# Performance work log

Hardware: AMD Instinct MI355X
Metric: run time of the kernel (lower is better)

Reference implementation:

```python
import jax, jax.numpy as jnp
import numpy as np

N_NODES = 100000
N_EDGES = 1600000
D_IN = 128
D_HID = 128
D_OUT = 128


def setup_inputs() -> dict:
    key = jax.random.key(0)
    ks = jax.random.split(key, 12)
    x = jax.random.normal(ks[0], (N_NODES, D_IN), dtype=jnp.float32)
    src = jax.random.randint(ks[1], (N_EDGES,), 0, N_NODES, dtype=jnp.int32)
    dst = jax.random.randint(ks[2], (N_EDGES,), 0, N_NODES, dtype=jnp.int32)
    s = 0.05
    # layer 0: in->hid, layer 1: hid->hid, layer 2: hid->out
    Wl0 = jax.random.normal(ks[3], (D_HID, D_IN), dtype=jnp.float32) * s
    bl0 = jnp.zeros((D_HID,), dtype=jnp.float32)
    Wr0 = jax.random.normal(ks[4], (D_HID, D_IN), dtype=jnp.float32) * s
    Wl1 = jax.random.normal(ks[5], (D_HID, D_HID), dtype=jnp.float32) * s
    bl1 = jnp.zeros((D_HID,), dtype=jnp.float32)
    Wr1 = jax.random.normal(ks[6], (D_HID, D_HID), dtype=jnp.float32) * s
    Wl2 = jax.random.normal(ks[7], (D_OUT, D_HID), dtype=jnp.float32) * s
    bl2 = jnp.zeros((D_OUT,), dtype=jnp.float32)
    Wr2 = jax.random.normal(ks[8], (D_OUT, D_HID), dtype=jnp.float32) * s
    return {"x": x, "src": src, "dst": dst,
            "Wl0": Wl0, "bl0": bl0, "Wr0": Wr0,
            "Wl1": Wl1, "bl1": bl1, "Wr1": Wr1,
            "Wl2": Wl2, "bl2": bl2, "Wr2": Wr2}


def _sage_conv(h, src, dst, Wl, bl, Wr, n_nodes):
    # mean aggregation over incoming neighbors: out_i = mean_{j: (j->i)} h_j
    msg = jax.ops.segment_sum(h[src], dst, num_segments=n_nodes)  # [N, d_in]
    deg = jax.ops.segment_sum(jnp.ones(dst.shape, dtype=h.dtype), dst, num_segments=n_nodes)
    agg = msg / jnp.maximum(deg, 1.0)[:, None]
    # PyG SAGEConv: lin_l(agg) (with bias) + lin_r(h) (root, no bias)
    return agg @ Wl.T + bl + h @ Wr.T


def reference(x, src, dst, Wl0, bl0, Wr0, Wl1, bl1, Wr1, Wl2, bl2, Wr2):
    n = x.shape[0]
    # dropout is identity in eval mode
    h = jax.nn.relu(_sage_conv(x, src, dst, Wl0, bl0, Wr0, n))
    h = jax.nn.relu(_sage_conv(h, src, dst, Wl1, bl1, Wr1, n))
    return _sage_conv(h, src, dst, Wl2, bl2, Wr2, n)
```

## Files before the change

kernel.cpp:

```cpp
#include <hip/hip_runtime.h>

#define N_NODES 100000
#define N_EDGES 1600000
#define D 128
#define NBS 98

typedef __attribute__((ext_vector_type(8))) short bf16x8;
typedef __attribute__((ext_vector_type(4))) float f32x4;
typedef __attribute__((ext_vector_type(4))) unsigned int u32x4;
typedef __attribute__((ext_vector_type(2))) unsigned int u32x2;

union U16x8 { u32x4 u; bf16x8 b; };

__device__ __forceinline__ unsigned int bf16_rne_hi(float x) {
    unsigned int u = __float_as_uint(x);
    unsigned int r = u + 0x7fffu + ((u >> 16) & 1u);
    return r & 0xffff0000u;
}
__device__ __forceinline__ unsigned int pack_hilo(float x) {
    unsigned int hb = bf16_rne_hi(x);
    float hf = __uint_as_float(hb);
    unsigned int lb = bf16_rne_hi(x - hf);
    return hb | (lb >> 16);
}
__device__ __forceinline__ float unpack_val(unsigned int p) {
    return __uint_as_float(p & 0xffff0000u) + __uint_as_float(p << 16);
}


__global__ __launch_bounds__(256) void hist_kernel(const int* __restrict__ dst,
                                                   int* __restrict__ cnt, int n) {
    int i = blockIdx.x * blockDim.x + threadIdx.x;
    if (i < n) atomicAdd(&cnt[dst[i]], 1);
}

__global__ __launch_bounds__(256) void scan_reduce(const int* __restrict__ cnt,
                                                   int* __restrict__ bsum, int n) {
    __shared__ int s[4];
    int b = blockIdx.x, t = threadIdx.x;
    int base = b * 1024;
    int v = 0;
    for (int q = 0; q < 4; ++q) {
        int i = base + q * 256 + t;
        if (i < n) v += cnt[i];
    }
    for (int off = 32; off > 0; off >>= 1) v += __shfl_down(v, off, 64);
    if ((t & 63) == 0) s[t >> 6] = v;
    __syncthreads();
    if (t == 0) bsum[b] = s[0] + s[1] + s[2] + s[3];
}

__global__ __launch_bounds__(128) void scan_partials(const int* __restrict__ bsum,
                                                     int* __restrict__ bpre) {
    __shared__ int s[128];
    int t = threadIdx.x;
    int v = (t < NBS) ? bsum[t] : 0;
    s[t] = v;
    __syncthreads();
    for (int off = 1; off < 128; off <<= 1) {
        int u = (t >= off) ? s[t - off] : 0;
        __syncthreads();
        s[t] += u;
        __syncthreads();
    }
    if (t < NBS) bpre[t] = s[t] - v;
}

__global__ __launch_bounds__(1024) void scan_write(const int* __restrict__ cnt,
                                                   const int* __restrict__ bpre,
                                                   int* __restrict__ row_ptr, int n) {
    __shared__ int s[1024];
    int b = blockIdx.x, t = threadIdx.x;
    int i = b * 1024 + t;
    int c = (i < n) ? cnt[i] : 0;
    s[t] = c;
    __syncthreads();
    for (int off = 1; off < 1024; off <<= 1) {
        int u = (t >= off) ? s[t - off] : 0;
        __syncthreads();
        s[t] += u;
        __syncthreads();
    }
    if (i < n) row_ptr[i] = bpre[b] + s[t] - c;
    if (b == 0 && t == 0) row_ptr[n] = N_EDGES;
}

__global__ __launch_bounds__(256) void scatter_kernel(const int* __restrict__ src,
                                                      const int* __restrict__ dst,
                                                      const int* __restrict__ row_ptr,
                                                      int* __restrict__ cursor,
                                                      int* __restrict__ sorted_src, int n) {
    int i = blockIdx.x * blockDim.x + threadIdx.x;
    if (i < n) {
        int d = dst[i];
        int p = atomicAdd(&cursor[d], 1);
        sorted_src[row_ptr[d] + p] = src[i];
    }
}


__global__ __launch_bounds__(256) void split_x(const float* __restrict__ x,
                                               unsigned int* __restrict__ Hp) {
    int i = blockIdx.x * 256 + threadIdx.x;
    if (i >= N_NODES * 32) return;
    float4 v = reinterpret_cast<const float4*>(x)[i];
    u32x4 p;
    p.x = pack_hilo(v.x); p.y = pack_hilo(v.y);
    p.z = pack_hilo(v.z); p.w = pack_hilo(v.w);
    *reinterpret_cast<u32x4*>(Hp + (size_t)i * 4) = p;
}

__global__ __launch_bounds__(256) void split_w(const float* __restrict__ Wl,
                                               const float* __restrict__ Wr,
                                               unsigned short* __restrict__ whi,
                                               unsigned short* __restrict__ wlo) {
    int i = blockIdx.x * 256 + threadIdx.x;
    if (i >= 128 * 256) return;
    int o = i >> 8, k = i & 255;
    float v = (k < 128) ? Wl[o * 128 + k] : Wr[o * 128 + (k - 128)];
    unsigned int hb = bf16_rne_hi(v);
    whi[i] = (unsigned short)(hb >> 16);
    wlo[i] = (unsigned short)(bf16_rne_hi(v - __uint_as_float(hb)) >> 16);
}


__global__ __launch_bounds__(256) void aggregate_packed(const unsigned int* __restrict__ Hp,
                                                        const int* __restrict__ row_ptr,
                                                        const int* __restrict__ sorted_src,
                                                        unsigned int* __restrict__ Ap) {
    int wid = (blockIdx.x * blockDim.x + threadIdx.x) >> 6;
    int lane = threadIdx.x & 63;
    if (wid >= N_NODES) return;
    int beg = row_ptr[wid], end = row_ptr[wid + 1];
    int deg = end - beg;
    float a0 = 0.f, a1 = 0.f;
    int j = beg;
    for (; j + 7 < end; j += 8) {
        int s0 = sorted_src[j + 0], s1 = sorted_src[j + 1];
        int s2 = sorted_src[j + 2], s3 = sorted_src[j + 3];
        int s4 = sorted_src[j + 4], s5 = sorted_src[j + 5];
        int s6 = sorted_src[j + 6], s7 = sorted_src[j + 7];
        u32x2 p0 = *reinterpret_cast<const u32x2*>(Hp + (size_t)s0 * D + lane * 2);
        u32x2 p1 = *reinterpret_cast<const u32x2*>(Hp + (size_t)s1 * D + lane * 2);
        u32x2 p2 = *reinterpret_cast<const u32x2*>(Hp + (size_t)s2 * D + lane * 2);
        u32x2 p3 = *reinterpret_cast<const u32x2*>(Hp + (size_t)s3 * D + lane * 2);
        u32x2 p4 = *reinterpret_cast<const u32x2*>(Hp + (size_t)s4 * D + lane * 2);
        u32x2 p5 = *reinterpret_cast<const u32x2*>(Hp + (size_t)s5 * D + lane * 2);
        u32x2 p6 = *reinterpret_cast<const u32x2*>(Hp + (size_t)s6 * D + lane * 2);
        u32x2 p7 = *reinterpret_cast<const u32x2*>(Hp + (size_t)s7 * D + lane * 2);
        a0 += unpack_val(p0.x) + unpack_val(p1.x) + unpack_val(p2.x) + unpack_val(p3.x)
            + unpack_val(p4.x) + unpack_val(p5.x) + unpack_val(p6.x) + unpack_val(p7.x);
        a1 += unpack_val(p0.y) + unpack_val(p1.y) + unpack_val(p2.y) + unpack_val(p3.y)
            + unpack_val(p4.y) + unpack_val(p5.y) + unpack_val(p6.y) + unpack_val(p7.y);
    }
    for (; j < end; ++j) {
        int s = sorted_src[j];
        u32x2 p = *reinterpret_cast<const u32x2*>(Hp + (size_t)s * D + lane * 2);
        a0 += unpack_val(p.x);
        a1 += unpack_val(p.y);
    }
    float inv = 1.0f / (float)max(deg, 1);
    u32x2 o;
    o.x = pack_hilo(a0 * inv);
    o.y = pack_hilo(a1 * inv);
    *reinterpret_cast<u32x2*>(Ap + (size_t)wid * D + lane * 2) = o;
}


__global__ __launch_bounds__(512, 2) void sage_gemm_mfma(
        const unsigned int* __restrict__ Hp,
        const unsigned int* __restrict__ Ap,
        const unsigned short* __restrict__ WHI,
        const unsigned short* __restrict__ WLO,
        const float* __restrict__ bl,
        void* __restrict__ outp,
        int relu, int pack_out) {
    __shared__ short WH[32768];
    __shared__ short WLl[32768];
    int tid = threadIdx.x;

    for (int i = tid; i < 4096; i += 512) {
        int o = i >> 5, kg = i & 31;
        int sk = (kg * 8) ^ ((o & 7) << 3);
        *reinterpret_cast<bf16x8*>(&WH[o * 256 + sk]) =
            *reinterpret_cast<const bf16x8*>(WHI + o * 256 + kg * 8);
        *reinterpret_cast<bf16x8*>(&WLl[o * 256 + sk]) =
            *reinterpret_cast<const bf16x8*>(WLO + o * 256 + kg * 8);
    }
    __syncthreads();

    int w = tid >> 6, l = tid & 63;
    int lr = l & 15, lg = l >> 4;
    int sw = (lr & 7) << 3;
    int mt0 = blockIdx.x * 256 + w * 32;
    int mt1 = mt0 + 16;
    int r0 = min(mt0 + lr, N_NODES - 1);
    int r1 = min(mt1 + lr, N_NODES - 1);
    const unsigned int* a0A = Ap + (size_t)r0 * D + lg * 8;
    const unsigned int* a0H = Hp + (size_t)r0 * D + lg * 8;
    const unsigned int* a1A = Ap + (size_t)r1 * D + lg * 8;
    const unsigned int* a1H = Hp + (size_t)r1 * D + lg * 8;

    f32x4 acc0[8], acc1[8];
    #pragma unroll
    for (int nt = 0; nt < 8; ++nt) { acc0[nt] = (f32x4)0.f; acc1[nt] = (f32x4)0.f; }

    u32x4 p00 = *reinterpret_cast<const u32x4*>(a0A);
    u32x4 p01 = *reinterpret_cast<const u32x4*>(a0A + 4);
    u32x4 p10 = *reinterpret_cast<const u32x4*>(a1A);
    u32x4 p11 = *reinterpret_cast<const u32x4*>(a1A + 4);

    #pragma unroll
    for (int kk = 0; kk < 8; ++kk) {
        U16x8 h0, l0, h1, l1;
        h0.u.x = (p00.x >> 16) | (p00.y & 0xffff0000u);
        l0.u.x = (p00.x & 0xffffu) | (p00.y << 16);
        h0.u.y = (p00.z >> 16) | (p00.w & 0xffff0000u);
        l0.u.y = (p00.z & 0xffffu) | (p00.w << 16);
        h0.u.z = (p01.x >> 16) | (p01.y & 0xffff0000u);
        l0.u.z = (p01.x & 0xffffu) | (p01.y << 16);
        h0.u.w = (p01.z >> 16) | (p01.w & 0xffff0000u);
        l0.u.w = (p01.z & 0xffffu) | (p01.w << 16);
        h1.u.x = (p10.x >> 16) | (p10.y & 0xffff0000u);
        l1.u.x = (p10.x & 0xffffu) | (p10.y << 16);
        h1.u.y = (p10.z >> 16) | (p10.w & 0xffff0000u);
        l1.u.y = (p10.z & 0xffffu) | (p10.w << 16);
        h1.u.z = (p11.x >> 16) | (p11.y & 0xffff0000u);
        l1.u.z = (p11.x & 0xffffu) | (p11.y << 16);
        h1.u.w = (p11.z >> 16) | (p11.w & 0xffff0000u);
        l1.u.w = (p11.z & 0xffffu) | (p11.w << 16);
        bf16x8 a0h = h0.b, a0l = l0.b, a1h = h1.b, a1l = l1.b;

        if (kk < 7) {
            int kn = kk + 1;
            const unsigned int* s0 = (kn < 4) ? (a0A + kn * 32) : (a0H + (kn - 4) * 32);
            const unsigned int* s1 = (kn < 4) ? (a1A + kn * 32) : (a1H + (kn - 4) * 32);
            p00 = *reinterpret_cast<const u32x4*>(s0);
            p01 = *reinterpret_cast<const u32x4*>(s0 + 4);
            p10 = *reinterpret_cast<const u32x4*>(s1);
            p11 = *reinterpret_cast<const u32x4*>(s1 + 4);
        }

        int ka = (kk * 32 + lg * 8) ^ sw;
        #pragma unroll
        for (int nt = 0; nt < 8; ++nt) {
            int base = nt * 4096 + lr * 256 + ka;
            bf16x8 bh = *reinterpret_cast<const bf16x8*>(WH + base);
            bf16x8 bl_ = *reinterpret_cast<const bf16x8*>(WLl + base);
            acc0[nt] = __builtin_amdgcn_mfma_f32_16x16x32_bf16(a0h, bh, acc0[nt], 0, 0, 0);
            acc0[nt] = __builtin_amdgcn_mfma_f32_16x16x32_bf16(a0l, bh, acc0[nt], 0, 0, 0);
            acc0[nt] = __builtin_amdgcn_mfma_f32_16x16x32_bf16(a0h, bl_, acc0[nt], 0, 0, 0);
            acc1[nt] = __builtin_amdgcn_mfma_f32_16x16x32_bf16(a1h, bh, acc1[nt], 0, 0, 0);
            acc1[nt] = __builtin_amdgcn_mfma_f32_16x16x32_bf16(a1l, bh, acc1[nt], 0, 0, 0);
            acc1[nt] = __builtin_amdgcn_mfma_f32_16x16x32_bf16(a1h, bl_, acc1[nt], 0, 0, 0);
        }
    }

    #pragma unroll
    for (int nt = 0; nt < 8; ++nt) {
        int col = nt * 16 + lr;
        float bv = bl[col];
        #pragma unroll
        for (int ri = 0; ri < 4; ++ri) {
            int n0 = mt0 + lg * 4 + ri;
            if (n0 < N_NODES) {
                float v = acc0[nt][ri] + bv;
                if (relu) v = fmaxf(v, 0.f);
                if (pack_out)
                    ((unsigned int*)outp)[(size_t)n0 * D + col] = pack_hilo(v);
                else
                    ((float*)outp)[(size_t)n0 * D + col] = v;
            }
            int n1 = mt1 + lg * 4 + ri;
            if (n1 < N_NODES) {
                float v = acc1[nt][ri] + bv;
                if (relu) v = fmaxf(v, 0.f);
                if (pack_out)
                    ((unsigned int*)outp)[(size_t)n1 * D + col] = pack_hilo(v);
                else
                    ((float*)outp)[(size_t)n1 * D + col] = v;
            }
        }
    }
}


extern "C" void kernel_launch(void* const* d_in, const int* in_sizes, int n_in,
                              void* d_out, int out_size, void* d_ws, size_t ws_size,
                              hipStream_t stream) {
    const float* x   = (const float*)d_in[0];
    const int*   src = (const int*)d_in[1];
    const int*   dst = (const int*)d_in[2];
    const float* Wl0 = (const float*)d_in[3];
    const float* bl0 = (const float*)d_in[4];
    const float* Wr0 = (const float*)d_in[5];
    const float* Wl1 = (const float*)d_in[6];
    const float* bl1 = (const float*)d_in[7];
    const float* Wr1 = (const float*)d_in[8];
    const float* Wl2 = (const float*)d_in[9];
    const float* bl2 = (const float*)d_in[10];
    const float* Wr2 = (const float*)d_in[11];

    int* cnt        = (int*)d_ws;
    int* row_ptr    = cnt + 100032;
    int* sorted_src = row_ptr + 100032;
    unsigned short* W0h = (unsigned short*)((char*)d_ws + 7200256);
    unsigned short* W0l = W0h + 32768;
    unsigned short* W1h = W0l + 32768;
    unsigned short* W1l = W1h + 32768;
    unsigned short* W2h = W1l + 32768;
    unsigned short* W2l = W2h + 32768;
    unsigned int* Ap = (unsigned int*)((char*)d_ws + 7593472);
    int* bsum = (int*)W0h;
    int* bpre = bsum + 128;

    unsigned int* Hp = (unsigned int*)d_out;
    float* outf = (float*)d_out;

    const int EB = (N_EDGES + 255) / 256;
    const int GB = (N_NODES + 255) / 256;
    const int AB = (N_NODES * 64 + 255) / 256;
    const int SB = (N_NODES * 32 + 255) / 256;
    const int WB = (128 * 256 + 255) / 256;

    hipMemsetAsync(cnt, 0, N_NODES * sizeof(int), stream);
    hist_kernel<<<EB, 256, 0, stream>>>(dst, cnt, N_EDGES);
    scan_reduce<<<NBS, 256, 0, stream>>>(cnt, bsum, N_NODES);
    scan_partials<<<1, 128, 0, stream>>>(bsum, bpre);
    scan_write<<<NBS, 1024, 0, stream>>>(cnt, bpre, row_ptr, N_NODES);
    hipMemsetAsync(cnt, 0, N_NODES * sizeof(int), stream);
    scatter_kernel<<<EB, 256, 0, stream>>>(src, dst, row_ptr, cnt, sorted_src, N_EDGES);

    split_x<<<SB, 256, 0, stream>>>(x, Hp);
    split_w<<<WB, 256, 0, stream>>>(Wl0, Wr0, W0h, W0l);
    split_w<<<WB, 256, 0, stream>>>(Wl1, Wr1, W1h, W1l);
    split_w<<<WB, 256, 0, stream>>>(Wl2, Wr2, W2h, W2l);

    aggregate_packed<<<AB, 256, 0, stream>>>(Hp, row_ptr, sorted_src, Ap);
    sage_gemm_mfma<<<GB, 512, 0, stream>>>(Hp, Ap, W0h, W0l, bl0, Hp, 1, 1);
    aggregate_packed<<<AB, 256, 0, stream>>>(Hp, row_ptr, sorted_src, Ap);
    sage_gemm_mfma<<<GB, 512, 0, stream>>>(Hp, Ap, W1h, W1l, bl1, Hp, 1, 1);
    aggregate_packed<<<AB, 256, 0, stream>>>(Hp, row_ptr, sorted_src, Ap);
    sage_gemm_mfma<<<GB, 512, 0, stream>>>(Hp, Ap, W2h, W2l, bl2, outf, 0, 0);
}
```

Measured before the change: 791.2 us.

## Use feature-chunked transposed layout for aggregation to improve gather cache locality

Stores node features in 16 column chunks of 8 packed values each, laid out chunk-major, and adds an aggregation kernel that stages each block's neighbor indices in shared memory and sweeps chunks one at a time. The aim is to keep each chunk's gather working set small enough to stay cache-resident instead of randomly gathering full rows from a large array. The GEMM kernel is templated to read and write the chunked layout. The new path needs a larger workspace and falls back to the old path otherwise. Gathers become narrower, 32-byte segments per neighbor, which may reduce memory efficiency.

```diff
diff --git a/kernel.cpp b/kernel.cpp
--- a/kernel.cpp
+++ b/kernel.cpp
@@ -4,6 +4,9 @@
 #define N_EDGES 1600000
 #define D 128
 #define NBS 98
+#define NCH 16
+#define CHW 8
+#define MAXE 2048
 
 typedef __attribute__((ext_vector_type(8))) short bf16x8;
 typedef __attribute__((ext_vector_type(4))) float f32x4;
@@ -98,17 +101,6 @@
     }
 }
 
-
-__global__ __launch_bounds__(256) void split_x(const float* __restrict__ x,
-                                               unsigned int* __restrict__ Hp) {
-    int i = blockIdx.x * 256 + threadIdx.x;
-    if (i >= N_NODES * 32) return;
-    float4 v = reinterpret_cast<const float4*>(x)[i];
-    u32x4 p;
-    p.x = pack_hilo(v.x); p.y = pack_hilo(v.y);
-    p.z = pack_hilo(v.z); p.w = pack_hilo(v.w);
-    *reinterpret_cast<u32x4*>(Hp + (size_t)i * 4) = p;
-}
 
 __global__ __launch_bounds__(256) void split_w(const float* __restrict__ Wl,
                                                const float* __restrict__ Wr,
@@ -121,6 +113,97 @@
     unsigned int hb = bf16_rne_hi(v);
     whi[i] = (unsigned short)(hb >> 16);
     wlo[i] = (unsigned short)(bf16_rne_hi(v - __uint_as_float(hb)) >> 16);
+}
+
+__global__ __launch_bounds__(256) void split_x_t(const float* __restrict__ x,
+                                                 unsigned int* __restrict__ Hpt) {
+    int i = blockIdx.x * 256 + threadIdx.x;
+    if (i >= N_NODES * NCH) return;
+    int n = i >> 4, c = i & 15;
+    float4 v0 = *reinterpret_cast<const float4*>(x + (size_t)n * D + c * CHW);
+    float4 v1 = *reinterpret_cast<const float4*>(x + (size_t)n * D + c * CHW + 4);
+    u32x4 p0, p1;
+    p0.x = pack_hilo(v0.x); p0.y = pack_hilo(v0.y);
+    p0.z = pack_hilo(v0.z); p0.w = pack_hilo(v0.w);
+    p1.x = pack_hilo(v1.x); p1.y = pack_hilo(v1.y);
+    p1.z = pack_hilo(v1.z); p1.w = pack_hilo(v1.w);
+    unsigned int* o = Hpt + ((size_t)c * N_NODES + n) * CHW;
+    *reinterpret_cast<u32x4*>(o) = p0;
+    *reinterpret_cast<u32x4*>(o + 4) = p1;
+}
+
+__global__ __launch_bounds__(256) void split_x(const float* __restrict__ x,
+                                               unsigned int* __restrict__ Hp) {
+    int i = blockIdx.x * 256 + threadIdx.x;
+    if (i >= N_NODES * 32) return;
+    float4 v = reinterpret_cast<const float4*>(x)[i];
+    u32x4 p;
+    p.x = pack_hilo(v.x); p.y = pack_hilo(v.y);
+    p.z = pack_hilo(v.z); p.w = pack_hilo(v.w);
+    *reinterpret_cast<u32x4*>(Hp + (size_t)i * 4) = p;
+}
+
+
+__global__ __launch_bounds__(512) void aggregate_chunked(
+        const unsigned int* __restrict__ Hpt,
+        const int* __restrict__ row_ptr,
+        const int* __restrict__ sorted_src,
+        unsigned int* __restrict__ Apt) {
+    __shared__ int ebeg[65];
+    __shared__ int eidx[MAXE];
+    int tid = threadIdx.x;
+    int node0 = blockIdx.x * 64;
+
+    if (tid < 65) ebeg[tid] = row_ptr[min(node0 + tid, N_NODES)];
+    __syncthreads();
+    int base = ebeg[0];
+    int total = ebeg[64] - base;
+    bool ov = total > MAXE;
+    if (!ov)
+        for (int i = tid; i < total; i += 512) eidx[i] = sorted_src[base + i];
+    __syncthreads();
+
+    int w = tid >> 6, lane = tid & 63;
+    int nl = w * 8 + (lane >> 3);
+    int d = lane & 7;
+    int node = node0 + nl;
+    bool valid = node < N_NODES;
+    int jb = ebeg[nl] - base;
+    int je = ebeg[nl + 1] - base;
+    float inv = 1.0f / (float)max(je - jb, 1);
+
+    for (int c = 0; c < NCH; ++c) {
+        const unsigned int* cb = Hpt + (size_t)c * N_NODES * CHW;
+        float acc = 0.f;
+        int j = jb;
+        if (!ov) {
+            for (; j + 7 < je; j += 8) {
+                int s0 = eidx[j + 0], s1 = eidx[j + 1], s2 = eidx[j + 2], s3 = eidx[j + 3];
+                int s4 = eidx[j + 4], s5 = eidx[j + 5], s6 = eidx[j + 6], s7 = eidx[j + 7];
+                unsigned int a0 = cb[(size_t)s0 * CHW + d];
+                unsigned int a1 = cb[(size_t)s1 * CHW + d];
+                unsigned int a2 = cb[(size_t)s2 * CHW + d];
+                unsigned int a3 = cb[(size_t)s3 * CHW + d];
+                unsigned int a4 = cb[(size_t)s4 * CHW + d];
+                unsigned int a5 = cb[(size_t)s5 * CHW + d];
+                unsigned int a6 = cb[(size_t)s6 * CHW + d];
+                unsigned int a7 = cb[(size_t)s7 * CHW + d];
+                acc += (unpack_val(a0) + unpack_val(a1)) + (unpack_val(a2) + unpack_val(a3))
+                     + ((unpack_val(a4) + unpack_val(a5)) + (unpack_val(a6) + unpack_val(a7)));
+            }
+            for (; j < je; ++j) {
+                unsigned int a = cb[(size_t)eidx[j] * CHW + d];
+                acc += unpack_val(a);
+            }
+        } else {
+            for (; j < je; ++j) {
+                int s = sorted_src[base + j];
+                acc += unpack_val(cb[(size_t)s * CHW + d]);
+            }
+        }
+        if (valid)
+            Apt[(size_t)c * N_NODES * CHW + (size_t)node * CHW + d] = pack_hilo(acc * inv);
+    }
 }
 
 
@@ -167,6 +250,7 @@
 }
 
 
+template<int TR>
 __global__ __launch_bounds__(512, 2) void sage_gemm_mfma(
         const unsigned int* __restrict__ Hp,
         const unsigned int* __restrict__ Ap,
@@ -196,10 +280,23 @@
     int mt1 = mt0 + 16;
     int r0 = min(mt0 + lr, N_NODES - 1);
     int r1 = min(mt1 + lr, N_NODES - 1);
-    const unsigned int* a0A = Ap + (size_t)r0 * D + lg * 8;
-    const unsigned int* a0H = Hp + (size_t)r0 * D + lg * 8;
-    const unsigned int* a1A = Ap + (size_t)r1 * D + lg * 8;
-    const unsigned int* a1H = Hp + (size_t)r1 * D + lg * 8;
+
+    const size_t STEP = (size_t)4 * N_NODES * CHW;
+    const unsigned int* a0A;
+    const unsigned int* a0H;
+    const unsigned int* a1A;
+    const unsigned int* a1H;
+    if (TR) {
+        a0A = Ap + ((size_t)lg * N_NODES + r0) * CHW;
+        a0H = Hp + ((size_t)lg * N_NODES + r0) * CHW;
+        a1A = Ap + ((size_t)lg * N_NODES + r1) * CHW;
+        a1H = Hp + ((size_t)lg * N_NODES + r1) * CHW;
+    } else {
+        a0A = Ap + (size_t)r0 * D + lg * 8;
+        a0H = Hp + (size_t)r0 * D + lg * 8;
+        a1A = Ap + (size_t)r1 * D + lg * 8;
+        a1H = Hp + (size_t)r1 * D + lg * 8;
+    }
 
     f32x4 acc0[8], acc1[8];
     #pragma unroll
@@ -233,8 +330,14 @@
 
         if (kk < 7) {
             int kn = kk + 1;
-            const unsigned int* s0 = (kn < 4) ? (a0A + kn * 32) : (a0H + (kn - 4) * 32);
-            const unsigned int* s1 = (kn < 4) ? (a1A + kn * 32) : (a1H + (kn - 4) * 32);
+            const unsigned int *s0, *s1;
+            if (TR) {
+                s0 = (kn < 4) ? (a0A + (size_t)kn * STEP) : (a0H + (size_t)(kn - 4) * STEP);
+                s1 = (kn < 4) ? (a1A + (size_t)kn * STEP) : (a1H + (size_t)(kn - 4) * STEP);
+            } else {
+                s0 = (kn < 4) ? (a0A + kn * 32) : (a0H + (kn - 4) * 32);
+                s1 = (kn < 4) ? (a1A + kn * 32) : (a1H + (kn - 4) * 32);
+            }
             p00 = *reinterpret_cast<const u32x4*>(s0);
             p01 = *reinterpret_cast<const u32x4*>(s0 + 4);
             p10 = *reinterpret_cast<const u32x4*>(s1);
@@ -266,18 +369,24 @@
             if (n0 < N_NODES) {
                 float v = acc0[nt][ri] + bv;
                 if (relu) v = fmaxf(v, 0.f);
-                if (pack_out)
-                    ((unsigned int*)outp)[(size_t)n0 * D + col] = pack_hilo(v);
-                else
+                if (pack_out) {
+                    if (TR)
+                        ((unsigned int*)outp)[((size_t)(col >> 3) * N_NODES + n0) * CHW + (col & 7)] = pack_hilo(v);
+                    else
+                        ((unsigned int*)outp)[(size_t)n0 * D + col] = pack_hilo(v);
+                } else
                     ((float*)outp)[(size_t)n0 * D + col] = v;
             }
             int n1 = mt1 + lg * 4 + ri;
             if (n1 < N_NODES) {
                 float v = acc1[nt][ri] + bv;
                 if (relu) v = fmaxf(v, 0.f);
-                if (pack_out)
-                    ((unsigned int*)outp)[(size_t)n1 * D + col] = pack_hilo(v);
-                else
+                if (pack_out) {
+                    if (TR)
+                        ((unsigned int*)outp)[((size_t)(col >> 3) * N_NODES + n1) * CHW + (col & 7)] = pack_hilo(v);
+                    else
+                        ((unsigned int*)outp)[(size_t)n1 * D + col] = pack_hilo(v);
+                } else
                     ((float*)outp)[(size_t)n1 * D + col] = v;
             }
         }
@@ -310,17 +419,11 @@
     unsigned short* W1l = W1h + 32768;
     unsigned short* W2h = W1l + 32768;
     unsigned short* W2l = W2h + 32768;
-    unsigned int* Ap = (unsigned int*)((char*)d_ws + 7593472);
     int* bsum = (int*)W0h;
     int* bpre = bsum + 128;
 
-    unsigned int* Hp = (unsigned int*)d_out;
-    float* outf = (float*)d_out;
-
     const int EB = (N_EDGES + 255) / 256;
     const int GB = (N_NODES + 255) / 256;
-    const int AB = (N_NODES * 64 + 255) / 256;
-    const int SB = (N_NODES * 32 + 255) / 256;
     const int WB = (128 * 256 + 255) / 256;
 
     hipMemsetAsync(cnt, 0, N_NODES * sizeof(int), stream);
@@ -331,15 +434,39 @@
     hipMemsetAsync(cnt, 0, N_NODES * sizeof(int), stream);
     scatter_kernel<<<EB, 256, 0, stream>>>(src, dst, row_ptr, cnt, sorted_src, N_EDGES);
 
-    split_x<<<SB, 256, 0, stream>>>(x, Hp);
     split_w<<<WB, 256, 0, stream>>>(Wl0, Wr0, W0h, W0l);
     split_w<<<WB, 256, 0, stream>>>(Wl1, Wr1, W1h, W1l);
     split_w<<<WB, 256, 0, stream>>>(Wl2, Wr2, W2h, W2l);
 
-    aggregate_packed<<<AB, 256, 0, stream>>>(Hp, row_ptr, sorted_src, Ap);
-    sage_gemm_mfma<<<GB, 512, 0, stream>>>(Hp, Ap, W0h, W0l, bl0, Hp, 1, 1);
-    aggregate_packed<<<AB, 256, 0, stream>>>(Hp, row_ptr, sorted_src, Ap);
-    sage_gemm_mfma<<<GB, 512, 0, stream>>>(Hp, Ap, W1h, W1l, bl1, Hp, 1, 1);
-    aggregate_packed<<<AB, 256, 0, stream>>>(Hp, row_ptr, sorted_src, Ap);
-    sage_gemm_mfma<<<GB, 512, 0, stream>>>(Hp, Ap, W2h, W2l, bl2, outf, 0, 0);
-}
+    if (ws_size >= 110000000ull) {
+        unsigned int* Hpt = (unsigned int*)((char*)d_ws + 7593472);
+        unsigned int* Apt = (unsigned int*)((char*)d_ws + 58793472);
+        float* outf = (float*)d_out;
+        const int SB = (N_NODES * NCH + 255) / 256;
+        const int AGB = (N_NODES + 63) / 64;
+
+        split_x_t<<<SB, 256, 0, stream>>>(x, Hpt);
+
+        aggregate_chunked<<<AGB, 512, 0, stream>>>(Hpt, row_ptr, sorted_src, Apt);
+        sage_gemm_mfma<1><<<GB, 512, 0, stream>>>(Hpt, Apt, W0h, W0l, bl0, Hpt, 1, 1);
+        aggregate_chunked<<<AGB, 512, 0, stream>>>(Hpt, row_ptr, sorted_src, Apt);
+        sage_gemm_mfma<1><<<GB, 512, 0, stream>>>(Hpt, Apt, W1h, W1l, bl1, Hpt, 1, 1);
+        aggregate_chunked<<<AGB, 512, 0, stream>>>(Hpt, row_ptr, sorted_src, Apt);
+        sage_gemm_mfma<1><<<GB, 512, 0, stream>>>(Hpt, Apt, W2h, W2l, bl2, outf, 0, 0);
+    } else {
+        unsigned int* Ap = (unsigned int*)((char*)d_ws + 7593472);
+        unsigned int* Hp = (unsigned int*)d_out;
+        float* outf = (float*)d_out;
+        const int SB = (N_NODES * 32 + 255) / 256;
+        const int AB = (N_NODES * 64 + 255) / 256;
+
+        split_x<<<SB, 256, 0, stream>>>(x, Hp);
+
+        aggregate_packed<<<AB, 256, 0, stream>>>(Hp, row_ptr, sorted_src, Ap);
+        sage_gemm_mfma<0><<<GB, 512, 0, stream>>>(Hp, Ap, W0h, W0l, bl0, Hp, 1, 1);
+        aggregate_packed<<<AB, 256, 0, stream>>>(Hp, row_ptr, sorted_src, Ap);
+        sage_gemm_mfma<0><<<GB, 512, 0, stream>>>(Hp, Ap, W1h, W1l, bl1, Hp, 1, 1);
+        aggregate_packed<<<AB, 256, 0, stream>>>(Hp, row_ptr, sorted_src, Ap);
+        sage_gemm_mfma<0><<<GB, 512, 0, stream>>>(Hp, Ap, W2h, W2l, bl2, outf, 0, 0);
+    }
+}
```

Result: slower. 1.380 ms (+74.4%).
